# Kernel optimization log

Measured on AMD Instinct MI355X. Metric: run time of the kernel, lower is better.

The kernel has to match this reference:

```python
import jax, jax.numpy as jnp
import numpy as np

B, S, D = 32, 1024, 1280          # batch, spatial tokens, hidden_size
CROSS = 768                        # cross_attention_dim
HEADS = 20
HD = D // HEADS                    # 64
N_AOE, N_IMG = 16, 16              # disease / anatomy token counts
SCALE = 1.0 / float(np.sqrt(HD))


def _split_heads(x):
    # [B, N, D] -> [B, H, N, HD]
    b, n, _ = x.shape
    return x.reshape(b, n, HEADS, HD).transpose(0, 2, 1, 3)


def _attend(q, k, v):
    # q: [B,H,S,HD], k/v: [B,H,K,HD]  (K is tiny, 16)
    scores = jnp.einsum('bhsd,bhkd->bhsk', q, k) * SCALE
    probs = jax.nn.softmax(scores, axis=-1)
    return jnp.einsum('bhsk,bhkd->bhsd', probs, v)


def setup_inputs() -> dict:
    key = jax.random.key(0)
    ks = jax.random.split(key, 10)
    g = lambda k, shape, sc=0.02: jax.random.normal(k, shape, jnp.float32) * sc
    return {
        'hidden_states': jax.random.normal(ks[0], (B, S, D), jnp.float32),
        'encoder_hidden_states': jax.random.normal(ks[1], (B, N_AOE + N_IMG + 16, CROSS), jnp.float32),
        'w_q': g(ks[2], (D, D)),            # attn.to_q, bias=False
        'w_k': g(ks[3], (D, CROSS)),        # attn.to_k (anatomy branch)
        'w_v': g(ks[4], (D, CROSS)),        # attn.to_v
        'w_k_dis': g(ks[5], (D, CROSS)),    # self.to_k_dis
        'w_v_dis': g(ks[6], (D, CROSS)),    # self.to_v_dis
        'w_gate': g(ks[7], (1, CROSS)),     # gate_modulator (randomized to exercise path; init is zeros)
        'b_gate': jnp.zeros((1,), jnp.float32),
        'anat_gate_logit': jnp.float32(0.0),  # logit(0.5) for block_type='both'
        'dis_gate_logit': jnp.float32(0.0),
        'w_out': g(ks[8], (D, D)),          # attn.to_out[0]
        'b_out': jnp.zeros((D,), jnp.float32),
    }


def reference(hidden_states, encoder_hidden_states, w_q, w_k, w_v, w_k_dis,
              w_v_dis, w_gate, b_gate, anat_gate_logit, dis_gate_logit,
              w_out, b_out):
    residual = hidden_states
    b = hidden_states.shape[0]

    # token splits (delta path disabled: delta_scale == 0.0)
    dis_tokens = encoder_hidden_states[:, :N_AOE, :]
    anat_tokens = encoder_hidden_states[:, N_AOE:N_AOE + N_IMG, :]

    # projections (torch Linear: x @ W^T)
    query = _split_heads(hidden_states @ w_q.T)          # [B,H,S,HD]
    k_anat = _split_heads(anat_tokens @ w_k.T)           # [B,H,16,HD]
    v_anat = _split_heads(anat_tokens @ w_v.T)
    k_dis = _split_heads(dis_tokens @ w_k_dis.T)
    v_dis = _split_heads(dis_tokens @ w_v_dis.T)

    z_anat = _attend(query, k_anat, v_anat)              # [B,H,S,HD]
    z_dis = _attend(query, k_dis, v_dis)

    # severity-driven gate shift
    severity = dis_tokens.mean(axis=1)                   # [B, CROSS]
    shift = (severity @ w_gate.T + b_gate).reshape(b, 1, 1, 1)
    anat_gate = jax.nn.sigmoid(anat_gate_logit - shift)
    dis_gate = jax.nn.sigmoid(dis_gate_logit + shift)

    z_final = anat_gate * z_anat + dis_gate * z_dis      # [B,H,S,HD]

    out = z_final.transpose(0, 2, 1, 3).reshape(b, -1, D)
    out = out @ w_out.T + b_out                          # to_out[0]; to_out[1] is dropout (eval identity)
    out = out + residual                                 # residual_connection=True, rescale_output_factor=1.0
    return out
```

## Files before the change

### kernel.cpp

```cpp
#include <hip/hip_runtime.h>
#include <stdint.h>

#define B_     32
#define S_     1024
#define D_     1280
#define CROSS_ 768
#define NTOK   16
#define SCALE_ 0.125f

typedef __bf16 bf16x8 __attribute__((ext_vector_type(8)));
typedef float  f32x4  __attribute__((ext_vector_type(4)));
typedef unsigned short ushort_t;
typedef unsigned int   uint_t;

__device__ __forceinline__ float b2f(ushort_t h){ return __uint_as_float(((uint_t)h)<<16); }
__device__ __forceinline__ ushort_t f2b(float f){
  uint_t u = __float_as_uint(f);
  u += 0x7FFFu + ((u>>16)&1u);
  return (ushort_t)(u>>16);
}
__device__ __forceinline__ uint_t pk2(float x, float y){
  return (uint_t)f2b(x) | ((uint_t)f2b(y)<<16);
}

__device__ __forceinline__ void gload_lds16(const void* g, void* l){
  __builtin_amdgcn_global_load_lds((const __attribute__((address_space(1))) void*)g,
                                   (__attribute__((address_space(3))) void*)l, 16, 0, 0);
}

struct CvtArgs { const float* src[7]; ushort_t* dst[7]; int n[7]; };
__global__ void cvt_kernel(CvtArgs a){
  int t = blockIdx.y;
  const float* s = a.src[t]; ushort_t* d = a.dst[t]; int n = a.n[t];
  int i = (blockIdx.x*blockDim.x + threadIdx.x)*4;
  if(i >= n) return;
  float4 v = *(const float4*)(s+i);
  uint2 o; o.x = pk2(v.x,v.y); o.y = pk2(v.z,v.w);
  *(uint2*)(d+i) = o;
}

__global__ void cvt_big(const float* __restrict__ s, ushort_t* __restrict__ d, int n){
  int i = (blockIdx.x*blockDim.x + threadIdx.x)*8;
  if(i >= n) return;
  float4 v0 = *(const float4*)(s+i), v1 = *(const float4*)(s+i+4);
  uint4 o = { pk2(v0.x,v0.y), pk2(v0.z,v0.w), pk2(v1.x,v1.y), pk2(v1.z,v1.w) };
  *(uint4*)(d+i) = o;
}

__global__ void gates_kernel(const float* __restrict__ enc,
                             const float* __restrict__ w_gate,
                             const float* __restrict__ b_gate,
                             const float* __restrict__ aLog,
                             const float* __restrict__ dLog,
                             float* __restrict__ gates){
  int b = blockIdx.x, tid = threadIdx.x;
  __shared__ float red[256];
  float acc = 0.f;
  for(int k = tid; k < CROSS_; k += 256){
    float s = 0.f;
    for(int t = 0; t < NTOK; ++t)
      s += enc[(size_t)(b*48 + t)*CROSS_ + k];
    acc += w_gate[k] * s;
  }
  red[tid] = acc; __syncthreads();
  for(int off = 128; off > 0; off >>= 1){
    if(tid < off) red[tid] += red[tid+off];
    __syncthreads();
  }
  if(tid == 0){
    float shift = red[0]*(1.f/16.f) + b_gate[0];
    gates[b*2+0] = 1.f/(1.f+__expf(shift - aLog[0]));
    gates[b*2+1] = 1.f/(1.f+__expf(-(dLog[0] + shift)));
  }
}

__global__ __launch_bounds__(256) void kv_gemm(const ushort_t* __restrict__ enc,
      const ushort_t* __restrict__ wk,  const ushort_t* __restrict__ wv,
      const ushort_t* __restrict__ wkd, const ushort_t* __restrict__ wvd,
      ushort_t* __restrict__ kv){
  __shared__ __align__(16) ushort_t As[128*64];
  __shared__ __align__(16) ushort_t Bs[128*64];
  const int tau = blockIdx.z;
  const ushort_t* W = (tau==0)? wk : (tau==1)? wv : (tau==2)? wkd : wvd;
  const int tok_off = (tau < 2) ? NTOK : 0;
  const int m0 = blockIdx.x*128, n0 = blockIdx.y*128;
  const int tid = threadIdx.x, l = tid & 63, w = tid >> 6;
  const int wm = (w&1)*64, wn = (w>>1)*64;
  const f32x4 fz = {0.f,0.f,0.f,0.f};
  f32x4 acc[4][4];
  #pragma unroll
  for(int i=0;i<4;++i){
    #pragma unroll
    for(int j=0;j<4;++j) acc[i][j] = fz;
  }
  for(int kt = 0; kt < CROSS_/64; ++kt){
    const int k0 = kt*64;
    #pragma unroll
    for(int i=0;i<4;++i){
      int row = (w*4+i)*8 + (l>>3);
      int c   = l & 7;
      int gm  = m0 + row;
      int er  = (gm>>4)*48 + tok_off + (gm&15);
      gload_lds16(enc + (size_t)er*CROSS_ + k0 + c*8, As + (w*4+i)*512);
      gload_lds16(W  + (size_t)(n0+row)*CROSS_ + k0 + c*8, Bs + (w*4+i)*512);
    }
    __syncthreads();
    #pragma unroll
    for(int ks = 0; ks < 64; ks += 32){
      bf16x8 a[4], bq[4];
      #pragma unroll
      for(int i=0;i<4;++i) a[i]  = *(const bf16x8*)&As[(wm+i*16+(l&15))*64 + ks + (l>>4)*8];
      #pragma unroll
      for(int j=0;j<4;++j) bq[j] = *(const bf16x8*)&Bs[(wn+j*16+(l&15))*64 + ks + (l>>4)*8];
      #pragma unroll
      for(int i=0;i<4;++i){
        #pragma unroll
        for(int j=0;j<4;++j)
          acc[i][j] = __builtin_amdgcn_mfma_f32_16x16x32_bf16(a[i], bq[j], acc[i][j], 0,0,0);
      }
    }
    __syncthreads();
  }
  #pragma unroll
  for(int i=0;i<4;++i){
    #pragma unroll
    for(int j=0;j<4;++j){
      #pragma unroll
      for(int r=0;r<4;++r){
        int m = m0 + wm + i*16 + (l>>4)*4 + r;
        int n = n0 + wn + j*16 + (l&15);
        int b = m >> 4, t = m & 15;
        kv[(((size_t)tau*B_ + b)*NTOK + t)*D_ + n] = f2b(acc[i][j][r]);
      }
    }
  }
}

#define VMW(n)  asm volatile("s_waitcnt vmcnt(" #n ")" ::: "memory")
#define FENCE() asm volatile("" ::: "memory")
#define BARX()  do{ FENCE(); __builtin_amdgcn_s_barrier(); FENCE(); }while(0)
#define LGKM0() asm volatile("s_waitcnt lgkmcnt(0)" ::: "memory")

__device__ __forceinline__ void stage_aq(const ushort_t* __restrict__ g,
                                         ushort_t* le, int tid){
  int row = tid >> 3;
  int c   = ((tid & 7) ^ (row & 7)) << 3;
  gload_lds16(g + (size_t)row*D_ + c, le + (tid>>6)*512);
}
__device__ __forceinline__ void stage_b2(const ushort_t* __restrict__ g,
                                         ushort_t* lh, int s0, int tid){
  int w   = tid >> 6;
  int blk = w >> 2;
  int t   = tid & 255;
  int rr  = s0 + blk*64 + (t >> 3);
  int c   = ((t & 7) ^ (rr & 7)) << 3;
  gload_lds16(g + (size_t)rr*D_ + c, lh + (s0 + blk*64)*64 + (w&3)*512);
}

#define AB(tt) (lds + ((tt)&1)*16384)
#define BB(tt) (lds + 32768 + ((tt)&1)*16384)
#define ST_S0(tt) { stage_aq(Asrc + (size_t)  0*D_ + (tt)*64, AB(tt),          tid); \
                    stage_aq(Asrc + (size_t)128*D_ + (tt)*64, AB(tt) + 8192,   tid); }
#define ST_S1(tt) { stage_b2(Bsrc + (size_t)  0*D_ + (tt)*64, BB(tt),        0, tid); \
                    stage_b2(Bsrc + (size_t)128*D_ + (tt)*64, BB(tt) + 8192, 0, tid); }
#define ST_S2(tt) { stage_b2(Bsrc + (size_t)  0*D_ + (tt)*64, BB(tt),       32, tid); \
                    stage_b2(Bsrc + (size_t)128*D_ + (tt)*64, BB(tt) + 8192,32, tid); }
#define ST_S3(tt) { stage_aq(Asrc + (size_t) 64*D_ + (tt)*64, AB(tt) + 4096,  tid); \
                    stage_aq(Asrc + (size_t)192*D_ + (tt)*64, AB(tt) + 12288, tid); }
#define DS_A(qi, Ab) { _Pragma("unroll") for(int i=0;i<4;++i){ \
      a[i][0] = *(const bf16x8*)&(Ab)[((qi)*64 + i*16 + lr)*64 + csw0]; \
      a[i][1] = *(const bf16x8*)&(Ab)[((qi)*64 + i*16 + lr)*64 + csw1]; } }
#define DS_B(qj, Bb) { _Pragma("unroll") for(int j=0;j<2;++j){ \
      bb[j][0] = *(const bf16x8*)&(Bb)[(bro + ((qj)*2+j)*16)*64 + csw0]; \
      bb[j][1] = *(const bf16x8*)&(Bb)[(bro + ((qj)*2+j)*16)*64 + csw1]; } }
#define MM(qi,qj) { __builtin_amdgcn_s_setprio(1); \
    _Pragma("unroll") for(int i=0;i<4;++i){ _Pragma("unroll") for(int j=0;j<2;++j){ \
      acc[(qi)*4+i][(qj)*2+j] = __builtin_amdgcn_mfma_f32_16x16x32_bf16(a[i][0], bb[j][0], acc[(qi)*4+i][(qj)*2+j],0,0,0); \
      acc[(qi)*4+i][(qj)*2+j] = __builtin_amdgcn_mfma_f32_16x16x32_bf16(a[i][1], bb[j][1], acc[(qi)*4+i][(qj)*2+j],0,0,0); } } \
    __builtin_amdgcn_s_setprio(0); }

#define MAINLOOP_256(NKT) \
  ST_S0(0); ST_S1(0); ST_S2(0); ST_S3(0); \
  VMW(4); \
  BARX(); \
  for(int t = 0; t < (NKT)-1; ++t){ \
    const ushort_t* Ab = AB(t) + wr*8192; \
    const ushort_t* Bb = BB(t) + (wc>>1)*8192; \
    DS_A(0,Ab); DS_B(0,Bb); ST_S0(t+1); VMW(4); BARX(); MM(0,0); BARX(); \
    DS_B(1,Bb);             ST_S1(t+1); VMW(4); BARX(); MM(0,1); BARX(); \
    DS_A(1,Ab); DS_B(0,Bb); ST_S2(t+1);         BARX(); MM(1,0); BARX(); \
    DS_B(1,Bb);             ST_S3(t+1); VMW(4); BARX(); MM(1,1); BARX(); \
  } \
  { \
    const ushort_t* Ab = AB((NKT)-1) + wr*8192; \
    const ushort_t* Bb = BB((NKT)-1) + (wc>>1)*8192; \
    DS_A(0,Ab); DS_B(0,Bb); VMW(2); BARX(); MM(0,0); BARX(); \
    DS_B(1,Bb);             VMW(0); BARX(); MM(0,1); BARX(); \
    DS_A(1,Ab); DS_B(0,Bb);         BARX(); MM(1,0); BARX(); \
    DS_B(1,Bb);                             MM(1,1); \
  }

__global__ __launch_bounds__(512,2) void gemm1_attn_8p(
      const ushort_t* __restrict__ X, const ushort_t* __restrict__ Wq,
      const ushort_t* __restrict__ kv, const float* __restrict__ gates,
      ushort_t* __restrict__ Z){
  __shared__ __align__(16) ushort_t lds[65536];
  const int lid = (blockIdx.x & 7)*80 + (blockIdx.x >> 3);
  const int m0 = (lid/5)*256, n0 = (lid%5)*256;
  const int tid = threadIdx.x, l = tid & 63, w = tid >> 6;
  const int wr = w >> 2, wc = w & 3;
  const int lr = l & 15;
  const int csw0 = ((l>>4)*8)    ^ ((l&7)<<3);
  const int csw1 = (32+(l>>4)*8) ^ ((l&7)<<3);
  const int bro  = (wc & 1)*64 + lr;
  const ushort_t* Asrc = X  + (size_t)m0*D_;
  const ushort_t* Bsrc = Wq + (size_t)n0*D_;
  const f32x4 fz = {0.f,0.f,0.f,0.f};
  f32x4 acc[8][4];
  #pragma unroll
  for(int i=0;i<8;++i){
    #pragma unroll
    for(int j=0;j<4;++j) acc[i][j] = fz;
  }
  bf16x8 a[4][2], bb[2][2];

  MAINLOOP_256(20)

  BARX();
  const int b = m0 >> 10;
  const float gA = gates[b*2+0], gD = gates[b*2+1];
  ushort_t* R = lds + w*8192;
  const ushort_t* kbase = kv + ((size_t)b*NTOK + lr)*D_ + n0 + wc*64 + (l>>4)*8;
  bf16x8 kA0 = *(const bf16x8*)(kbase);
  bf16x8 kA1 = *(const bf16x8*)(kbase + 32);
  bf16x8 kD0 = *(const bf16x8*)(kbase + (size_t)2*B_*NTOK*D_);
  bf16x8 kD1 = *(const bf16x8*)(kbase + (size_t)2*B_*NTOK*D_ + 32);
  f32x4 scA[8], scD[8];
  #pragma unroll
  for(int i=0;i<8;++i){ scA[i] = fz; scD[i] = fz; }
  #pragma unroll
  for(int i=0;i<8;++i){
    ushort_t* qs = R + (i&1)*1024;
    #pragma unroll
    for(int j=0;j<4;++j){
      #pragma unroll
      for(int r=0;r<4;++r){
        int row = (l>>4)*4 + r;
        int col = j*16 + lr;
        qs[row*64 + ((((col>>3) ^ (row&7))<<3) | (col&7))] = f2b(acc[i][j][r]);
      }
    }
    LGKM0();
    bf16x8 af0 = *(const bf16x8*)&qs[lr*64 + ((((l>>4))   ^ (lr&7))<<3)];
    bf16x8 af1 = *(const bf16x8*)&qs[lr*64 + (((4+(l>>4)) ^ (lr&7))<<3)];
    scA[i] = __builtin_amdgcn_mfma_f32_16x16x32_bf16(af0, kA0, scA[i], 0,0,0);
    scA[i] = __builtin_amdgcn_mfma_f32_16x16x32_bf16(af1, kA1, scA[i], 0,0,0);
    scD[i] = __builtin_amdgcn_mfma_f32_16x16x32_bf16(af0, kD0, scD[i], 0,0,0);
    scD[i] = __builtin_amdgcn_mfma_f32_16x16x32_bf16(af1, kD1, scD[i], 0,0,0);
  }
  uint4 vld[4];
  #pragma unroll
  for(int it=0; it<4; ++it){
    int u = it*64 + l;
    int tp = u >> 3, c = u & 7;
    int tensor = (tp < 16) ? 1 : 3;
    int t = tp & 15;
    vld[it] = *(const uint4*)(kv + (((size_t)tensor*B_ + b)*NTOK + t)*D_
                                 + n0 + wc*64 + c*8);
  }
  LGKM0();
  #pragma unroll
  for(int i=0;i<8;++i){
    #pragma unroll
    for(int r=0;r<4;++r){
      float vA = scA[i][r]*SCALE_, vD = scD[i][r]*SCALE_;
      float mA = vA, mD = vD;
      #pragma unroll
      for(int off=1; off<16; off<<=1){
        mA = fmaxf(mA, __shfl_xor(mA, off));
        mD = fmaxf(mD, __shfl_xor(mD, off));
      }
      float eA = __expf(vA - mA), eD = __expf(vD - mD);
      float sA = eA, sD = eD;
      #pragma unroll
      for(int off=1; off<16; off<<=1){
        sA += __shfl_xor(sA, off);
        sD += __shfl_xor(sD, off);
      }
      int lrow = i*16 + (l>>4)*4 + r;
      R[lrow*44 + lr]      = f2b(gA*eA/sA);
      R[lrow*44 + 16 + lr] = f2b(gD*eD/sD);
    }
  }
  ushort_t* vts = R + 5632;
  #pragma unroll
  for(int it=0; it<4; ++it){
    int u = it*64 + l;
    int tp = u >> 3, c = u & 7;
    const ushort_t* pv = (const ushort_t*)&vld[it];
    #pragma unroll
    for(int e=0;e<8;++e) vts[(c*8+e)*40 + tp] = pv[e];
  }
  LGKM0();
  bf16x8 pa[8], vb[4];
  #pragma unroll
  for(int i=0;i<8;++i) pa[i] = *(const bf16x8*)&R[(i*16+lr)*44 + (l>>4)*8];
  #pragma unroll
  for(int j=0;j<4;++j)  vb[j] = *(const bf16x8*)&vts[(j*16+lr)*40 + (l>>4)*8];
  f32x4 z[8][4];
  #pragma unroll
  for(int i=0;i<8;++i){
    #pragma unroll
    for(int j=0;j<4;++j)
      z[i][j] = __builtin_amdgcn_mfma_f32_16x16x32_bf16(pa[i], vb[j], fz, 0,0,0);
  }
  #pragma unroll
  for(int i=0;i<8;++i){
    #pragma unroll
    for(int j=0;j<4;++j){
      #pragma unroll
      for(int r=0;r<4;++r){
        int row = m0 + wr*128 + i*16 + (l>>4)*4 + r;
        int col = n0 + wc*64 + j*16 + lr;
        Z[(size_t)row*D_ + col] = f2b(z[i][j][r]);
      }
    }
  }
}

__global__ __launch_bounds__(512,2) void gemm2_8p(
      const ushort_t* __restrict__ Zin, const ushort_t* __restrict__ Wo,
      const float* __restrict__ bias, const float* __restrict__ resid,
      float* __restrict__ out){
  __shared__ __align__(16) ushort_t lds[65536];
  const int lid = (blockIdx.x & 7)*80 + (blockIdx.x >> 3);
  const int m0 = (lid/5)*256, n0 = (lid%5)*256;
  const int tid = threadIdx.x, l = tid & 63, w = tid >> 6;
  const int wr = w >> 2, wc = w & 3;
  const int lr = l & 15;
  const int csw0 = ((l>>4)*8)    ^ ((l&7)<<3);
  const int csw1 = (32+(l>>4)*8) ^ ((l&7)<<3);
  const int bro  = (wc & 1)*64 + lr;
  const ushort_t* Asrc = Zin + (size_t)m0*D_;
  const ushort_t* Bsrc = Wo  + (size_t)n0*D_;
  const f32x4 fz = {0.f,0.f,0.f,0.f};
  f32x4 acc[8][4];
  #pragma unroll
  for(int i=0;i<8;++i){
    #pragma unroll
    for(int j=0;j<4;++j) acc[i][j] = fz;
  }
  bf16x8 a[4][2], bb[2][2];

  MAINLOOP_256(20)

  float bj[4];
  #pragma unroll
  for(int j=0;j<4;++j) bj[j] = bias[n0 + wc*64 + j*16 + lr];
  #pragma unroll
  for(int i=0;i<8;++i){
    #pragma unroll
    for(int j=0;j<4;++j){
      #pragma unroll
      for(int r=0;r<4;++r){
        int m = m0 + wr*128 + i*16 + (l>>4)*4 + r;
        int n = n0 + wc*64 + j*16 + lr;
        out[(size_t)m*D_ + n] = acc[i][j][r] + bj[j] + resid[(size_t)m*D_ + n];
      }
    }
  }
}

extern "C" void kernel_launch(void* const* d_in, const int* in_sizes, int n_in,
                              void* d_out, int out_size, void* d_ws, size_t ws_size,
                              hipStream_t stream){
  const float* hidden = (const float*)d_in[0];
  const float* enc    = (const float*)d_in[1];
  const float* w_q    = (const float*)d_in[2];
  const float* w_k    = (const float*)d_in[3];
  const float* w_v    = (const float*)d_in[4];
  const float* w_kd   = (const float*)d_in[5];
  const float* w_vd   = (const float*)d_in[6];
  const float* w_gate = (const float*)d_in[7];
  const float* b_gate = (const float*)d_in[8];
  const float* aLog   = (const float*)d_in[9];
  const float* dLog   = (const float*)d_in[10];
  const float* w_out  = (const float*)d_in[11];
  const float* b_out  = (const float*)d_in[12];
  float* out = (float*)d_out;

  char* ws = (char*)d_ws;
  ushort_t* z_bf   = (ushort_t*)(ws + 0);
  ushort_t* kv_bf  = (ushort_t*)(ws + 83886080);
  ushort_t* wq_bf  = (ushort_t*)(ws + 89128960);
  ushort_t* wk_bf  = (ushort_t*)(ws + 92405760);
  ushort_t* wv_bf  = (ushort_t*)(ws + 94371840);
  ushort_t* wkd_bf = (ushort_t*)(ws + 96337920);
  ushort_t* wvd_bf = (ushort_t*)(ws + 98304000);
  ushort_t* wo_bf  = (ushort_t*)(ws + 100270080);
  ushort_t* enc_bf = (ushort_t*)(ws + 103546880);
  float*    gates  = (float*)   (ws + 105906176);

  ushort_t* hid_bf = (ushort_t*)d_out;

  CvtArgs ca;
  ca.src[0]=w_q;   ca.dst[0]=wq_bf;  ca.n[0]=D_*D_;
  ca.src[1]=w_k;   ca.dst[1]=wk_bf;  ca.n[1]=D_*CROSS_;
  ca.src[2]=w_v;   ca.dst[2]=wv_bf;  ca.n[2]=D_*CROSS_;
  ca.src[3]=w_kd;  ca.dst[3]=wkd_bf; ca.n[3]=D_*CROSS_;
  ca.src[4]=w_vd;  ca.dst[4]=wvd_bf; ca.n[4]=D_*CROSS_;
  ca.src[5]=w_out; ca.dst[5]=wo_bf;  ca.n[5]=D_*D_;
  ca.src[6]=enc;   ca.dst[6]=enc_bf; ca.n[6]=B_*48*CROSS_;
  cvt_kernel<<<dim3(1600,7), 256, 0, stream>>>(ca);
  cvt_big<<<20480, 256, 0, stream>>>(hidden, hid_bf, B_*S_*D_);

  gates_kernel<<<32, 256, 0, stream>>>(enc, w_gate, b_gate, aLog, dLog, gates);
  kv_gemm<<<dim3(4,10,4), 256, 0, stream>>>(enc_bf, wk_bf, wv_bf, wkd_bf, wvd_bf, kv_bf);
  gemm1_attn_8p<<<640, 512, 0, stream>>>(hid_bf, wq_bf, kv_bf, gates, z_bf);
  gemm2_8p<<<640, 512, 0, stream>>>(z_bf, wo_bf, b_out, hidden, out);
}
```

Before: 666.4 us.

## Triple-buffer A tiles with two-tile-ahead prefetch in both GEMM main loops

Both GEMM main loops change from double-buffering A and B to triple-buffering the A operand (X or Z tiles) while keeping B double-buffered. A tiles are now prefetched two K-steps ahead and B tiles one step ahead, with wait counts and the peeled epilogue iterations adjusted to match. The intent is to hide more global-to-LDS latency behind the MFMA work. In exchange, each block's LDS grows to 160KB, which uses the whole CU LDS and rules out any co-resident block, and the loop is unrolled by six, which adds code size.

```diff
diff --git a/kernel.cpp b/kernel.cpp
--- a/kernel.cpp
+++ b/kernel.cpp
@@ -157,16 +157,16 @@
   gload_lds16(g + (size_t)rr*D_ + c, lh + (s0 + blk*64)*64 + (w&3)*512);
 }
 
-#define AB(tt) (lds + ((tt)&1)*16384)
-#define BB(tt) (lds + 32768 + ((tt)&1)*16384)
-#define ST_S0(tt) { stage_aq(Asrc + (size_t)  0*D_ + (tt)*64, AB(tt),          tid); \
-                    stage_aq(Asrc + (size_t)128*D_ + (tt)*64, AB(tt) + 8192,   tid); }
-#define ST_S1(tt) { stage_b2(Bsrc + (size_t)  0*D_ + (tt)*64, BB(tt),        0, tid); \
-                    stage_b2(Bsrc + (size_t)128*D_ + (tt)*64, BB(tt) + 8192, 0, tid); }
-#define ST_S2(tt) { stage_b2(Bsrc + (size_t)  0*D_ + (tt)*64, BB(tt),       32, tid); \
-                    stage_b2(Bsrc + (size_t)128*D_ + (tt)*64, BB(tt) + 8192,32, tid); }
-#define ST_S3(tt) { stage_aq(Asrc + (size_t) 64*D_ + (tt)*64, AB(tt) + 4096,  tid); \
-                    stage_aq(Asrc + (size_t)192*D_ + (tt)*64, AB(tt) + 12288, tid); }
+#define A3(s) (lds + (s)*16384)
+#define B2(u) (lds + 49152 + (u)*16384)
+#define ST_GA0(tt,s) { stage_aq(Asrc + (size_t)  0*D_ + (tt)*64, A3(s),          tid); \
+                       stage_aq(Asrc + (size_t)128*D_ + (tt)*64, A3(s) + 8192,   tid); }
+#define ST_GA1(tt,s) { stage_aq(Asrc + (size_t) 64*D_ + (tt)*64, A3(s) + 4096,   tid); \
+                       stage_aq(Asrc + (size_t)192*D_ + (tt)*64, A3(s) + 12288,  tid); }
+#define ST_GB0(tt,u) { stage_b2(Bsrc + (size_t)  0*D_ + (tt)*64, B2(u),        0, tid); \
+                       stage_b2(Bsrc + (size_t)128*D_ + (tt)*64, B2(u) + 8192, 0, tid); }
+#define ST_GB1(tt,u) { stage_b2(Bsrc + (size_t)  0*D_ + (tt)*64, B2(u),       32, tid); \
+                       stage_b2(Bsrc + (size_t)128*D_ + (tt)*64, B2(u) + 8192,32, tid); }
 #define DS_A(qi, Ab) { _Pragma("unroll") for(int i=0;i<4;++i){ \
       a[i][0] = *(const bf16x8*)&(Ab)[((qi)*64 + i*16 + lr)*64 + csw0]; \
       a[i][1] = *(const bf16x8*)&(Ab)[((qi)*64 + i*16 + lr)*64 + csw1]; } }
@@ -179,23 +179,37 @@
       acc[(qi)*4+i][(qj)*2+j] = __builtin_amdgcn_mfma_f32_16x16x32_bf16(a[i][1], bb[j][1], acc[(qi)*4+i][(qj)*2+j],0,0,0); } } \
     __builtin_amdgcn_s_setprio(0); }
 
-#define MAINLOOP_256(NKT) \
-  ST_S0(0); ST_S1(0); ST_S2(0); ST_S3(0); \
-  VMW(4); \
+#define TILE_N(t, s_cur, s_pf2, u_cur, u_nx) { \
+    const ushort_t* Ab = A3(s_cur) + wr*8192; \
+    const ushort_t* Bb = B2(u_cur) + (wc>>1)*8192; \
+    DS_A(0,Ab); DS_B(0,Bb); ST_GB0((t)+1,u_nx); VMW(6); BARX(); MM(0,0); BARX(); \
+    DS_B(1,Bb);             ST_GB1((t)+1,u_nx);         BARX(); MM(0,1); BARX(); \
+    DS_A(1,Ab); DS_B(0,Bb); ST_GA0((t)+2,s_pf2);        BARX(); MM(1,0); BARX(); \
+    DS_B(1,Bb);             ST_GA1((t)+2,s_pf2); VMW(6); BARX(); MM(1,1); BARX(); }
+
+#define MAINLOOP4 \
+  ST_GA0(0,0); ST_GA1(0,0); ST_GB0(0,0); ST_GB1(0,0); ST_GA0(1,1); ST_GA1(1,1); \
+  VMW(6); \
   BARX(); \
-  for(int t = 0; t < (NKT)-1; ++t){ \
-    const ushort_t* Ab = AB(t) + wr*8192; \
-    const ushort_t* Bb = BB(t) + (wc>>1)*8192; \
-    DS_A(0,Ab); DS_B(0,Bb); ST_S0(t+1); VMW(4); BARX(); MM(0,0); BARX(); \
-    DS_B(1,Bb);             ST_S1(t+1); VMW(4); BARX(); MM(0,1); BARX(); \
-    DS_A(1,Ab); DS_B(0,Bb); ST_S2(t+1);         BARX(); MM(1,0); BARX(); \
-    DS_B(1,Bb);             ST_S3(t+1); VMW(4); BARX(); MM(1,1); BARX(); \
+  for(int tt6 = 0; tt6 < 18; tt6 += 6){ \
+    _Pragma("unroll") \
+    for(int uu = 0; uu < 6; ++uu){ \
+      TILE_N(tt6+uu, (uu%3), ((uu+2)%3), (uu&1), ((uu+1)&1)); \
+    } \
   } \
-  { \
-    const ushort_t* Ab = AB((NKT)-1) + wr*8192; \
-    const ushort_t* Bb = BB((NKT)-1) + (wc>>1)*8192; \
-    DS_A(0,Ab); DS_B(0,Bb); VMW(2); BARX(); MM(0,0); BARX(); \
-    DS_B(1,Bb);             VMW(0); BARX(); MM(0,1); BARX(); \
+  {  \
+    const ushort_t* Ab = A3(0) + wr*8192; \
+    const ushort_t* Bb = B2(0) + (wc>>1)*8192; \
+    DS_A(0,Ab); DS_B(0,Bb); ST_GB0(19,1); VMW(6); BARX(); MM(0,0); BARX(); \
+    DS_B(1,Bb);             ST_GB1(19,1);         BARX(); MM(0,1); BARX(); \
+    DS_A(1,Ab); DS_B(0,Bb);                       BARX(); MM(1,0); BARX(); \
+    DS_B(1,Bb);                           VMW(2); BARX(); MM(1,1); BARX(); \
+  } \
+  {  \
+    const ushort_t* Ab = A3(1) + wr*8192; \
+    const ushort_t* Bb = B2(1) + (wc>>1)*8192; \
+    DS_A(0,Ab); DS_B(0,Bb); VMW(0); BARX(); MM(0,0); BARX(); \
+    DS_B(1,Bb);                     BARX(); MM(0,1); BARX(); \
     DS_A(1,Ab); DS_B(0,Bb);         BARX(); MM(1,0); BARX(); \
     DS_B(1,Bb);                             MM(1,1); \
   }
@@ -204,7 +218,7 @@
       const ushort_t* __restrict__ X, const ushort_t* __restrict__ Wq,
       const ushort_t* __restrict__ kv, const float* __restrict__ gates,
       ushort_t* __restrict__ Z){
-  __shared__ __align__(16) ushort_t lds[65536];
+  __shared__ __align__(16) ushort_t lds[81920];
   const int lid = (blockIdx.x & 7)*80 + (blockIdx.x >> 3);
   const int m0 = (lid/5)*256, n0 = (lid%5)*256;
   const int tid = threadIdx.x, l = tid & 63, w = tid >> 6;
@@ -224,7 +238,7 @@
   }
   bf16x8 a[4][2], bb[2][2];
 
-  MAINLOOP_256(20)
+  MAINLOOP4
 
   BARX();
   const int b = m0 >> 10;
@@ -332,7 +346,7 @@
       const ushort_t* __restrict__ Zin, const ushort_t* __restrict__ Wo,
       const float* __restrict__ bias, const float* __restrict__ resid,
       float* __restrict__ out){
-  __shared__ __align__(16) ushort_t lds[65536];
+  __shared__ __align__(16) ushort_t lds[81920];
   const int lid = (blockIdx.x & 7)*80 + (blockIdx.x >> 3);
   const int m0 = (lid/5)*256, n0 = (lid%5)*256;
   const int tid = threadIdx.x, l = tid & 63, w = tid >> 6;
@@ -352,7 +366,7 @@
   }
   bf16x8 a[4][2], bb[2][2];
 
-  MAINLOOP_256(20)
+  MAINLOOP4
 
   float bj[4];
   #pragma unroll
```

Result: no change. 656.6 us (-1.5%).
